# Kernel tuning notes

Measured on AMD Instinct MI355X. Metric: run time of the kernel, lower is better.

Reference implementation:

```python
import jax, jax.numpy as jnp
import numpy as np

B, T, S, H, E = 128, 32, 256, 1024, 1024


def setup_inputs() -> dict:
    key = jax.random.key(0)
    ks = jax.random.split(key, 8)
    sc = lambda n: 1.0 / np.sqrt(n)
    return dict(
        dec_seq=jax.random.normal(ks[0], (B, T, E), jnp.float32),      # embedded decoder inputs
        enc_hiddens=jax.random.normal(ks[1], (B, S, H), jnp.float32),  # encoder outputs
        last_hidden=jax.random.normal(ks[2], (B, H), jnp.float32),     # initial decoder state
        W_att=jax.random.normal(ks[3], (2 * H, H), jnp.float32) * sc(2 * H),  # concat-score W
        V_att=jax.random.normal(ks[4], (H, 1), jnp.float32) * sc(H),          # concat-score V
        Wi=jax.random.normal(ks[5], (E + H, 3 * H), jnp.float32) * sc(E + H),  # GRU input kernel (z,r,h)
        Uh=jax.random.normal(ks[6], (H, 3 * H), jnp.float32) * sc(H),          # GRU recurrent kernel
        b=jnp.zeros((3 * H,), jnp.float32),                                    # GRU bias
    )


def reference(dec_seq, enc_hiddens, last_hidden, W_att, V_att, Wi, Uh, b):
    Bn, Sn, Hn = enc_hiddens.shape

    def step(h, x_t):
        # Bahdanau 'concat' score: tanh([h; enc] @ W) @ V -> softmax over source
        hid = jnp.broadcast_to(h[:, None, :], (Bn, Sn, Hn))
        combined = jnp.concatenate([hid, enc_hiddens], axis=2)          # [B,S,2H]
        score = jnp.tanh(jnp.einsum('bsk,kh->bsh', combined, W_att))    # [B,S,H]
        score = jnp.einsum('bsh,h->bs', score, V_att[:, 0])             # [B,S]
        attn = jax.nn.softmax(score, axis=-1)
        context = jnp.einsum('bs,bsh->bh', attn, enc_hiddens)           # [B,H]
        # GRU cell on concat([x_t, context])
        inp = jnp.concatenate([x_t, context], axis=1)                   # [B,E+H]
        gz, gr, gh = jnp.split(inp @ Wi + b, 3, axis=1)
        rz, rr, rh = jnp.split(h @ Uh, 3, axis=1)
        z = jax.nn.sigmoid(gz + rz)
        r = jax.nn.sigmoid(gr + rr)
        hh = jnp.tanh(gh + r * rh)
        h_new = z * h + (1.0 - z) * hh
        return h_new, h_new

    _, outs = jax.lax.scan(step, last_hidden, jnp.swapaxes(dec_seq, 0, 1))
    return jnp.swapaxes(outs, 0, 1)  # [B,T,H]
```

## Files before the change

### kernel.cpp

```cpp
#include <hip/hip_runtime.h>
#include <hip/hip_bf16.h>
#include <stdint.h>

#define B_ 128
#define T_ 32
#define S_ 256
#define H_ 1024
#define E_ 1024
#define LOG2E 1.4426950408889634f

typedef __attribute__((ext_vector_type(8))) short short8;
typedef __attribute__((ext_vector_type(4))) float f32x4;
typedef __attribute__((ext_vector_type(2))) float f32x2;

typedef const __attribute__((address_space(1))) unsigned int* gas_ptr;
typedef __attribute__((address_space(3))) unsigned int* las_ptr;

__device__ __forceinline__ void gl_lds16(const void* g, void* l) {
    __builtin_amdgcn_global_load_lds((gas_ptr)g, (las_ptr)l, 16, 0, 0);
}

__device__ __forceinline__ float bf2f(unsigned short u) {
    union { unsigned int i; float f; } v; v.i = ((unsigned int)u) << 16; return v.f;
}
__device__ __forceinline__ unsigned short f2bf(float f) {
    union { float f; unsigned int i; } v; v.f = f;
    unsigned int i = v.i;
    return (unsigned short)((i + 0x7FFFu + ((i >> 16) & 1u)) >> 16);
}
__device__ __forceinline__ unsigned char f2fp8(float f) {
    return (unsigned char)((unsigned int)__builtin_amdgcn_cvt_pk_fp8_f32(f, f, 0, false) & 0xFF);
}
__device__ __forceinline__ float fexp2(float x) { return __builtin_amdgcn_exp2f(x); }
__device__ __forceinline__ float frcp(float x)  { return __builtin_amdgcn_rcpf(x); }
__device__ __forceinline__ float fast_tanh(float x) {
    float e = fexp2(x * (2.0f * LOG2E));
    return 1.0f - 2.0f * frcp(e + 1.0f);
}
__device__ __forceinline__ float fast_sigmoid(float x) {
    return frcp(1.0f + fexp2(-LOG2E * x));
}

__global__ __launch_bounds__(256) void conv_bf16(const float* __restrict__ src,
                                                 unsigned short* __restrict__ dst, long n) {
    long i = ((long)blockIdx.x * 256 + threadIdx.x) * 8;
    if (i >= n) return;
    float4 x = *(const float4*)(src + i);
    float4 y = *(const float4*)(src + i + 4);
    unsigned int w0 = (unsigned int)f2bf(x.x) | ((unsigned int)f2bf(x.y) << 16);
    unsigned int w1 = (unsigned int)f2bf(x.z) | ((unsigned int)f2bf(x.w) << 16);
    unsigned int w2 = (unsigned int)f2bf(y.x) | ((unsigned int)f2bf(y.y) << 16);
    unsigned int w3 = (unsigned int)f2bf(y.z) | ((unsigned int)f2bf(y.w) << 16);
    uint4 o; o.x = w0; o.y = w1; o.z = w2; o.w = w3;
    *(uint4*)(dst + i) = o;
}

__global__ __launch_bounds__(256) void conv_fp8(const float* __restrict__ src,
                                                unsigned char* __restrict__ dst, long n) {
    long i = ((long)blockIdx.x * 256 + threadIdx.x) * 8;
    if (i >= n) return;
    float4 x = *(const float4*)(src + i);
    float4 y = *(const float4*)(src + i + 4);
    unsigned int w0 = (unsigned int)__builtin_amdgcn_cvt_pk_fp8_f32(x.x, x.y, 0, false);
    w0 = (unsigned int)__builtin_amdgcn_cvt_pk_fp8_f32(x.z, x.w, (int)w0, true);
    unsigned int w1 = (unsigned int)__builtin_amdgcn_cvt_pk_fp8_f32(y.x, y.y, 0, false);
    w1 = (unsigned int)__builtin_amdgcn_cvt_pk_fp8_f32(y.z, y.w, (int)w1, true);
    uint2 o; o.x = w0; o.y = w1;
    *(uint2*)(dst + i) = o;
}

__global__ __launch_bounds__(256) void init_h(const float* __restrict__ h0,
                                              float* __restrict__ hbuf,
                                              unsigned short* __restrict__ hbf, int n) {
    int i = blockIdx.x * 256 + threadIdx.x;
    if (i < n) { float v = h0[i]; hbuf[i] = v; hbf[i] = f2bf(v); }
}

__global__ __launch_bounds__(256) void transpose_conv(const float* __restrict__ src, int ldsrc,
                                                      unsigned short* __restrict__ dst, int lddst,
                                                      float scale) {
    __shared__ float tile[64][65];
    int tid = threadIdx.x;
    int c0 = blockIdx.x * 64, r0 = blockIdx.y * 64;
    int tr = tid >> 6, tc = tid & 63;
#pragma unroll
    for (int i = 0; i < 16; i++) {
        int r = i * 4 + tr;
        tile[r][tc] = src[(long)(r0 + r) * ldsrc + c0 + tc];
    }
    __syncthreads();
#pragma unroll
    for (int i = 0; i < 16; i++) {
        int rr = i * 4 + tr;
        dst[(long)(c0 + rr) * lddst + r0 + tc] = f2bf(scale * tile[tc][rr]);
    }
}

__global__ __launch_bounds__(256) void transpose_conv_fp8(const float* __restrict__ src, int ldsrc,
                                                          unsigned char* __restrict__ dst, int lddst,
                                                          float scale) {
    __shared__ float tile[64][65];
    int tid = threadIdx.x;
    int c0 = blockIdx.x * 64, r0 = blockIdx.y * 64;
    int tr = tid >> 6, tc = tid & 63;
#pragma unroll
    for (int i = 0; i < 16; i++) {
        int r = i * 4 + tr;
        tile[r][tc] = src[(long)(r0 + r) * ldsrc + c0 + tc];
    }
    __syncthreads();
#pragma unroll
    for (int i = 0; i < 16; i++) {
        int rr = i * 4 + tr;
        dst[(long)(c0 + rr) * lddst + r0 + tc] = f2fp8(scale * tile[tc][rr]);
    }
}

template <int EPIL, int SWZ>
__global__ __launch_bounds__(256) void gemm128(const unsigned short* __restrict__ A, int lda,
                                               const unsigned short* __restrict__ Bt, int ldb,
                                               void* __restrict__ Cout, int ldc,
                                               int kLen, long partStride) {
    __shared__ unsigned short As[128 * 32];
    __shared__ unsigned short Bs[128 * 32];
    const int tid = threadIdx.x;
    int lin = blockIdx.y * gridDim.x + blockIdx.x;
    if (SWZ) {
        int cpx = (gridDim.x * gridDim.y) >> 3;
        lin = (lin & 7) * cpx + (lin >> 3);
    }
    const int n0 = (lin % gridDim.x) * 128;
    const int m0 = (lin / gridDim.x) * 128;
    const int kStart = blockIdx.z * kLen;
    const int w = tid >> 6, l = tid & 63;
    const int wr = w >> 1, wc = w & 1;

    f32x4 acc[4][4];
#pragma unroll
    for (int i = 0; i < 4; i++)
#pragma unroll
        for (int j = 0; j < 4; j++) acc[i][j] = f32x4{0.f, 0.f, 0.f, 0.f};

    for (int kt = 0; kt < kLen; kt += 32) {
        int k0 = kStart + kt;
#pragma unroll
        for (int i = 0; i < 2; i++) {
            int f = i * 4096 + tid * 16;
            int row = f >> 6;
            int cb = f & 63;
            gl_lds16(A + (long)(m0 + row) * lda + k0 + (cb >> 1), (char*)As + f);
            gl_lds16(Bt + (long)(n0 + row) * ldb + k0 + (cb >> 1), (char*)Bs + f);
        }
        asm volatile("s_waitcnt vmcnt(0)" ::: "memory");
        __syncthreads();
        short8 a[4], b[4];
#pragma unroll
        for (int fi = 0; fi < 4; fi++) {
            a[fi] = *(const short8*)((const char*)As + ((wr * 64 + fi * 16 + (l & 15)) * 32 + ((l >> 4) * 8)) * 2);
            b[fi] = *(const short8*)((const char*)Bs + ((wc * 64 + fi * 16 + (l & 15)) * 32 + ((l >> 4) * 8)) * 2);
        }
#pragma unroll
        for (int fi = 0; fi < 4; fi++)
#pragma unroll
            for (int fj = 0; fj < 4; fj++)
                acc[fi][fj] = __builtin_amdgcn_mfma_f32_16x16x32_bf16(a[fi], b[fj], acc[fi][fj], 0, 0, 0);
        __syncthreads();
    }

    long cz = (long)blockIdx.z * partStride;
#pragma unroll
    for (int fi = 0; fi < 4; fi++)
#pragma unroll
        for (int fj = 0; fj < 4; fj++) {
            int m = m0 + wr * 64 + fi * 16 + ((l >> 4) << 2);
            int n = n0 + wc * 64 + fj * 16 + (l & 15);
#pragma unroll
            for (int r = 0; r < 4; r++)
                ((unsigned short*)Cout + cz)[(long)(m + r) * ldc + n] = f2bf(acc[fi][fj][r]);
        }
}

template <int SWZ>
__global__ __launch_bounds__(256) void gemm128_f8(const unsigned char* __restrict__ A, int lda,
                                                  const unsigned char* __restrict__ Bt, int ldb,
                                                  unsigned char* __restrict__ Cout, int ldc,
                                                  int kLen) {
    __shared__ unsigned char As[128 * 64];
    __shared__ unsigned char Bs[128 * 64];
    const int tid = threadIdx.x;
    int lin = blockIdx.y * gridDim.x + blockIdx.x;
    if (SWZ) {
        int cpx = (gridDim.x * gridDim.y) >> 3;
        lin = (lin & 7) * cpx + (lin >> 3);
    }
    const int n0 = (lin % gridDim.x) * 128;
    const int m0 = (lin / gridDim.x) * 128;
    const int w = tid >> 6, l = tid & 63;
    const int wr = w >> 1, wc = w & 1;
    const int sx = (l & 6) << 3;

    f32x4 acc[4][4];
#pragma unroll
    for (int i = 0; i < 4; i++)
#pragma unroll
        for (int j = 0; j < 4; j++) acc[i][j] = f32x4{0.f, 0.f, 0.f, 0.f};

    for (int k0 = 0; k0 < kLen; k0 += 64) {
#pragma unroll
        for (int i = 0; i < 2; i++) {
            int f = i * 4096 + tid * 16;
            int row = f >> 6;
            int cb = (f & 63) ^ ((row & 6) << 3);
            gl_lds16(A + (long)(m0 + row) * lda + k0 + cb, (char*)As + f);
            gl_lds16(Bt + (long)(n0 + row) * ldb + k0 + cb, (char*)Bs + f);
        }
        asm volatile("s_waitcnt vmcnt(0)" ::: "memory");
        __syncthreads();
        long a[4][2], b[4][2];
#pragma unroll
        for (int fi = 0; fi < 4; fi++)
#pragma unroll
            for (int ks = 0; ks < 2; ks++) {
                int colb = (ks * 32 + ((l >> 4) * 8)) ^ sx;
                a[fi][ks] = *(const long*)(As + (wr * 64 + fi * 16 + (l & 15)) * 64 + colb);
                b[fi][ks] = *(const long*)(Bs + (wc * 64 + fi * 16 + (l & 15)) * 64 + colb);
            }
#pragma unroll
        for (int fi = 0; fi < 4; fi++)
#pragma unroll
            for (int fj = 0; fj < 4; fj++) {
                acc[fi][fj] = __builtin_amdgcn_mfma_f32_16x16x32_fp8_fp8(a[fi][0], b[fj][0], acc[fi][fj], 0, 0, 0);
                acc[fi][fj] = __builtin_amdgcn_mfma_f32_16x16x32_fp8_fp8(a[fi][1], b[fj][1], acc[fi][fj], 0, 0, 0);
            }
        __syncthreads();
    }

#pragma unroll
    for (int fi = 0; fi < 4; fi++)
#pragma unroll
        for (int fj = 0; fj < 4; fj++) {
            int m = m0 + wr * 64 + fi * 16 + ((l >> 4) << 2);
            int n = n0 + wc * 64 + fj * 16 + (l & 15);
#pragma unroll
            for (int r = 0; r < 4; r++)
                Cout[(long)(m + r) * ldc + n] = f2fp8(acc[fi][fj][r]);
        }
}

__global__ __launch_bounds__(256) void recgates(const unsigned short* __restrict__ hbf,
                                                const unsigned short* __restrict__ ctxbf,
                                                const unsigned short* __restrict__ Uht,
                                                const unsigned short* __restrict__ Wit2,
                                                unsigned short* __restrict__ gpart) {
    __shared__ unsigned short As[128 * 32];
    __shared__ unsigned short Bs[128 * 32];
    const int tid = threadIdx.x;
    const int n0 = blockIdx.x * 128;
    const int y = blockIdx.y, z = blockIdx.z;
    const unsigned short* A  = y ? ctxbf : hbf;
    const unsigned short* Bt = y ? Wit2 : Uht;
    const int kStart = z * 256;
    const int w = tid >> 6, l = tid & 63;
    const int wr = w >> 1, wc = w & 1;

    f32x4 acc[4][4];
#pragma unroll
    for (int i = 0; i < 4; i++)
#pragma unroll
        for (int j = 0; j < 4; j++) acc[i][j] = f32x4{0.f, 0.f, 0.f, 0.f};

    for (int kt = 0; kt < 256; kt += 32) {
        int k0 = kStart + kt;
#pragma unroll
        for (int i = 0; i < 2; i++) {
            int f = i * 4096 + tid * 16;
            int row = f >> 6;
            int cb = f & 63;
            gl_lds16(A + (long)row * 1024 + k0 + (cb >> 1), (char*)As + f);
            gl_lds16(Bt + (long)(n0 + row) * 1024 + k0 + (cb >> 1), (char*)Bs + f);
        }
        asm volatile("s_waitcnt vmcnt(0)" ::: "memory");
        __syncthreads();
        short8 a[4], b[4];
#pragma unroll
        for (int fi = 0; fi < 4; fi++) {
            a[fi] = *(const short8*)((const char*)As + ((wr * 64 + fi * 16 + (l & 15)) * 32 + ((l >> 4) * 8)) * 2);
            b[fi] = *(const short8*)((const char*)Bs + ((wc * 64 + fi * 16 + (l & 15)) * 32 + ((l >> 4) * 8)) * 2);
        }
#pragma unroll
        for (int fi = 0; fi < 4; fi++)
#pragma unroll
            for (int fj = 0; fj < 4; fj++)
                acc[fi][fj] = __builtin_amdgcn_mfma_f32_16x16x32_bf16(a[fi], b[fj], acc[fi][fj], 0, 0, 0);
        __syncthreads();
    }

    unsigned short* C = gpart + (long)(y * 4 + z) * (128 * 3072);
#pragma unroll
    for (int fi = 0; fi < 4; fi++)
#pragma unroll
        for (int fj = 0; fj < 4; fj++) {
            int m = wr * 64 + fi * 16 + ((l >> 4) << 2);
            int n = n0 + wc * 64 + fj * 16 + (l & 15);
#pragma unroll
            for (int r = 0; r < 4; r++)
                C[(long)(m + r) * 3072 + n] = f2bf(acc[fi][fj][r]);
        }
}

__global__ __launch_bounds__(256) void attn_kernel(const unsigned char* __restrict__ P8,
                                                   const unsigned char* __restrict__ enc8,
                                                   const unsigned short* __restrict__ partq,
                                                   const float* __restrict__ V,
                                                   float* __restrict__ pctx,
                                                   float* __restrict__ pml) {
    const int oct = blockIdx.x, b = blockIdx.y;
    const int tid = threadIdx.x, w = tid >> 6, l = tid & 63;
    __shared__ float qs[1024];
    __shared__ float sc[32];
    __shared__ float wgt[32];

    {
        int j = tid * 4;
        float s0 = 0.f, s1 = 0.f, s2 = 0.f, s3 = 0.f;
#pragma unroll
        for (int p = 0; p < 8; p++) {
            ushort4 v = *(const ushort4*)(partq + (long)p * (128 * 1024) + (long)b * 1024 + j);
            s0 += bf2f(v.x); s1 += bf2f(v.y); s2 += bf2f(v.z); s3 += bf2f(v.w);
        }
        qs[j] = s0; qs[j + 1] = s1; qs[j + 2] = s2; qs[j + 3] = s3;
    }
    __syncthreads();

    float q[16], nv2[16];
    float sv = 0.f;
#pragma unroll
    for (int ii = 0; ii < 4; ii++) {
        float4 qq = *(const float4*)(qs + l * 16 + ii * 4);
        float4 vv = *(const float4*)(V + l * 16 + ii * 4);
        q[ii * 4 + 0] = qq.x; q[ii * 4 + 1] = qq.y; q[ii * 4 + 2] = qq.z; q[ii * 4 + 3] = qq.w;
        nv2[ii * 4 + 0] = -2.f * vv.x; nv2[ii * 4 + 1] = -2.f * vv.y;
        nv2[ii * 4 + 2] = -2.f * vv.z; nv2[ii * 4 + 3] = -2.f * vv.w;
        sv += vv.x + vv.y + vv.z + vv.w;
    }

    const int s0 = oct * 32;
#pragma unroll 2
    for (int ss = 0; ss < 8; ss++) {
        int s = w * 8 + ss;
        const unsigned char* prow = P8 + ((long)(b * S_ + s0 + s)) * H_ + l * 16;
        uint4 pw = *(const uint4*)prow;
        float pv[16];
        {
            f32x2 d;
            d = __builtin_amdgcn_cvt_pk_f32_fp8(pw.x, false); pv[0] = d.x; pv[1] = d.y;
            d = __builtin_amdgcn_cvt_pk_f32_fp8(pw.x, true);  pv[2] = d.x; pv[3] = d.y;
            d = __builtin_amdgcn_cvt_pk_f32_fp8(pw.y, false); pv[4] = d.x; pv[5] = d.y;
            d = __builtin_amdgcn_cvt_pk_f32_fp8(pw.y, true);  pv[6] = d.x; pv[7] = d.y;
            d = __builtin_amdgcn_cvt_pk_f32_fp8(pw.z, false); pv[8] = d.x; pv[9] = d.y;
            d = __builtin_amdgcn_cvt_pk_f32_fp8(pw.z, true);  pv[10] = d.x; pv[11] = d.y;
            d = __builtin_amdgcn_cvt_pk_f32_fp8(pw.w, false); pv[12] = d.x; pv[13] = d.y;
            d = __builtin_amdgcn_cvt_pk_f32_fp8(pw.w, true);  pv[14] = d.x; pv[15] = d.y;
        }
        float acc = sv;
#pragma unroll
        for (int i = 0; i < 16; i++) {
            float x = q[i] + pv[i];
            float d = frcp(fexp2(x) + 1.0f);
            acc = fmaf(d, nv2[i], acc);
        }
#pragma unroll
        for (int off = 32; off; off >>= 1) acc += __shfl_xor(acc, off);
        if (l == 0) sc[s] = acc;
    }
    __syncthreads();

    float v = (l < 32) ? sc[l] : -3.4e38f;
    float mx = v;
#pragma unroll
    for (int off = 32; off; off >>= 1) mx = fmaxf(mx, __shfl_xor(mx, off));
    float ex = (l < 32) ? fexp2((v - mx) * LOG2E) : 0.f;
    float ls = ex;
#pragma unroll
    for (int off = 32; off; off >>= 1) ls += __shfl_xor(ls, off);
    if (tid < 32) wgt[tid] = ex;
    if (tid == 0) {
        pml[(oct * 128 + b) * 2 + 0] = mx;
        pml[(oct * 128 + b) * 2 + 1] = ls;
    }
    __syncthreads();

    float a0 = 0.f, a1 = 0.f, a2 = 0.f, a3 = 0.f;
    const unsigned char* ebase = enc8 + ((long)(b * S_ + s0)) * H_ + tid * 4;
#pragma unroll 4
    for (int s = 0; s < 32; s++) {
        float ws = wgt[s];
        unsigned int u = *(const unsigned int*)(ebase + (long)s * H_);
        f32x2 lo = __builtin_amdgcn_cvt_pk_f32_fp8(u, false);
        f32x2 hi = __builtin_amdgcn_cvt_pk_f32_fp8(u, true);
        a0 = fmaf(ws, lo.x, a0);
        a1 = fmaf(ws, lo.y, a1);
        a2 = fmaf(ws, hi.x, a2);
        a3 = fmaf(ws, hi.y, a3);
    }
    float* po = pctx + ((long)(oct * 128 + b)) * H_ + tid * 4;
    po[0] = a0; po[1] = a1; po[2] = a2; po[3] = a3;
}

__global__ __launch_bounds__(256) void combine_ctx(const float* __restrict__ pctx,
                                                   const float* __restrict__ pml,
                                                   unsigned short* __restrict__ ctxbf) {
    int b = blockIdx.x, tid = threadIdx.x;
    float mm[8], ll[8];
    float m = -3.4e38f;
#pragma unroll
    for (int p = 0; p < 8; p++) {
        mm[p] = pml[(p * 128 + b) * 2 + 0];
        ll[p] = pml[(p * 128 + b) * 2 + 1];
        m = fmaxf(m, mm[p]);
    }
    float denom = 0.f, f[8];
#pragma unroll
    for (int p = 0; p < 8; p++) { f[p] = fexp2((mm[p] - m) * LOG2E); denom += f[p] * ll[p]; }
    float inv = frcp(denom);
    float a0 = 0.f, a1 = 0.f, a2 = 0.f, a3 = 0.f;
#pragma unroll
    for (int p = 0; p < 8; p++) {
        float4 c = *(const float4*)(pctx + ((long)(p * 128 + b)) * H_ + tid * 4);
        a0 = fmaf(f[p], c.x, a0); a1 = fmaf(f[p], c.y, a1);
        a2 = fmaf(f[p], c.z, a2); a3 = fmaf(f[p], c.w, a3);
    }
    unsigned short* o = ctxbf + (long)b * H_ + tid * 4;
    o[0] = f2bf(a0 * inv); o[1] = f2bf(a1 * inv); o[2] = f2bf(a2 * inv); o[3] = f2bf(a3 * inv);
}

__global__ __launch_bounds__(256) void gru_update(const unsigned short* __restrict__ gpart,
                                                  const unsigned short* __restrict__ xg,
                                                  const float* __restrict__ bias,
                                                  float* __restrict__ hbuf,
                                                  unsigned short* __restrict__ hbf,
                                                  float* __restrict__ out, int t) {
    const int m = blockIdx.x;
    const int j = threadIdx.x * 4;
    const unsigned short* xr = xg + ((long)(m * T_ + t)) * 3072;
    ushort4 xz = *(const ushort4*)(xr + j);
    ushort4 xrr = *(const ushort4*)(xr + 1024 + j);
    ushort4 xh = *(const ushort4*)(xr + 2048 + j);
    float gz[4] = {bf2f(xz.x), bf2f(xz.y), bf2f(xz.z), bf2f(xz.w)};
    float gr[4] = {bf2f(xrr.x), bf2f(xrr.y), bf2f(xrr.z), bf2f(xrr.w)};
    float gh[4] = {bf2f(xh.x), bf2f(xh.y), bf2f(xh.z), bf2f(xh.w)};
    float rz[4] = {0, 0, 0, 0}, rr[4] = {0, 0, 0, 0}, rh[4] = {0, 0, 0, 0};
#pragma unroll
    for (int p = 0; p < 8; p++) {
        const unsigned short* gp = gpart + (long)p * (128 * 3072) + (long)m * 3072;
        ushort4 a = *(const ushort4*)(gp + j);
        ushort4 bb = *(const ushort4*)(gp + 1024 + j);
        ushort4 c = *(const ushort4*)(gp + 2048 + j);
        if (p < 4) {
            rz[0] += bf2f(a.x); rz[1] += bf2f(a.y); rz[2] += bf2f(a.z); rz[3] += bf2f(a.w);
            rr[0] += bf2f(bb.x); rr[1] += bf2f(bb.y); rr[2] += bf2f(bb.z); rr[3] += bf2f(bb.w);
            rh[0] += bf2f(c.x); rh[1] += bf2f(c.y); rh[2] += bf2f(c.z); rh[3] += bf2f(c.w);
        } else {
            gz[0] += bf2f(a.x); gz[1] += bf2f(a.y); gz[2] += bf2f(a.z); gz[3] += bf2f(a.w);
            gr[0] += bf2f(bb.x); gr[1] += bf2f(bb.y); gr[2] += bf2f(bb.z); gr[3] += bf2f(bb.w);
            gh[0] += bf2f(c.x); gh[1] += bf2f(c.y); gh[2] += bf2f(c.z); gh[3] += bf2f(c.w);
        }
    }
    float4 bz = *(const float4*)(bias + j);
    float4 br = *(const float4*)(bias + 1024 + j);
    float4 bh = *(const float4*)(bias + 2048 + j);
    float4 hv = *(const float4*)(hbuf + (long)m * H_ + j);
    float bzf[4] = {bz.x, bz.y, bz.z, bz.w};
    float brf[4] = {br.x, br.y, br.z, br.w};
    float bhf[4] = {bh.x, bh.y, bh.z, bh.w};
    float hf[4] = {hv.x, hv.y, hv.z, hv.w};
    float hn[4];
    ushort4 hb;
#pragma unroll
    for (int c = 0; c < 4; c++) {
        float z = fast_sigmoid(gz[c] + bzf[c] + rz[c]);
        float r = fast_sigmoid(gr[c] + brf[c] + rr[c]);
        float hh = fast_tanh(gh[c] + bhf[c] + r * rh[c]);
        hn[c] = z * hf[c] + (1.0f - z) * hh;
    }
    hb.x = f2bf(hn[0]); hb.y = f2bf(hn[1]); hb.z = f2bf(hn[2]); hb.w = f2bf(hn[3]);
    float4 ho; ho.x = hn[0]; ho.y = hn[1]; ho.z = hn[2]; ho.w = hn[3];
    *(float4*)(out + ((long)m * T_ + t) * H_ + j) = ho;
    *(float4*)(hbuf + (long)m * H_ + j) = ho;
    *(ushort4*)(hbf + (long)m * H_ + j) = hb;
}

__global__ void sentinel_k(float* out) {
    if (threadIdx.x == 0 && blockIdx.x == 0) out[0] = 1.2345e8f;
}

extern "C" void kernel_launch(void* const* d_in, const int* in_sizes, int n_in,
                              void* d_out, int out_size, void* d_ws, size_t ws_size,
                              hipStream_t stream) {
    const float* dec  = (const float*)d_in[0];
    const float* enc  = (const float*)d_in[1];
    const float* h0   = (const float*)d_in[2];
    const float* Watt = (const float*)d_in[3];
    const float* Vatt = (const float*)d_in[4];
    const float* Wi   = (const float*)d_in[5];
    const float* Uh   = (const float*)d_in[6];
    const float* bias = (const float*)d_in[7];
    float* out = (float*)d_out;

    char* ws = (char*)d_ws;
    size_t off = 0;
    auto alloc = [&](size_t bytes) -> void* {
        void* p = ws + off;
        off += (bytes + 255) & ~(size_t)255;
        return p;
    };
    unsigned char*  P8    = (unsigned char*)alloc((size_t)32768 * 1024);
    unsigned char*  enc8  = (unsigned char*)alloc((size_t)33554432);
    unsigned short* decbf = (unsigned short*)alloc((size_t)4194304 * 2);
    unsigned short* Xg    = (unsigned short*)alloc((size_t)4096 * 3072 * 2);
    unsigned short* Wit1  = (unsigned short*)alloc((size_t)3072 * 1024 * 2);
    unsigned short* Wit2  = (unsigned short*)alloc((size_t)3072 * 1024 * 2);
    unsigned short* Uht   = (unsigned short*)alloc((size_t)3072 * 1024 * 2);
    unsigned short* W1t   = (unsigned short*)alloc((size_t)1024 * 1024 * 2);
    unsigned char*  W2t8  = (unsigned char*)alloc((size_t)1024 * 1024);
    unsigned short* partq = (unsigned short*)alloc((size_t)8 * 128 * 1024 * 2);
    unsigned short* gpart = (unsigned short*)alloc((size_t)8 * 128 * 3072 * 2);
    float* pctx  = (float*)alloc((size_t)8 * 128 * 1024 * 4);
    float* pml   = (float*)alloc((size_t)8 * 128 * 2 * 4);
    unsigned short* ctxbf = (unsigned short*)alloc((size_t)128 * 1024 * 2);
    float* hbuf  = (float*)alloc((size_t)128 * 1024 * 4);
    unsigned short* hbf = (unsigned short*)alloc((size_t)128 * 1024 * 2);

    if (off > ws_size) {
        sentinel_k<<<1, 64, 0, stream>>>(out);
        return;
    }

    const float qscale = 2.0f * LOG2E;

    conv_fp8<<<33554432 / 8 / 256, 256, 0, stream>>>(enc, enc8, 33554432);
    conv_bf16<<<4194304 / 8 / 256, 256, 0, stream>>>(dec, decbf, 4194304);
    init_h<<<512, 256, 0, stream>>>(h0, hbuf, hbf, 131072);
    transpose_conv<<<dim3(48, 16), 256, 0, stream>>>(Wi, 3072, Wit1, 1024, 1.0f);
    transpose_conv<<<dim3(48, 16), 256, 0, stream>>>(Wi + (size_t)1024 * 3072, 3072, Wit2, 1024, 1.0f);
    transpose_conv<<<dim3(48, 16), 256, 0, stream>>>(Uh, 3072, Uht, 1024, 1.0f);
    transpose_conv<<<dim3(16, 16), 256, 0, stream>>>(Watt, 1024, W1t, 1024, qscale);
    transpose_conv_fp8<<<dim3(16, 16), 256, 0, stream>>>(Watt + (size_t)1024 * 1024, 1024, W2t8, 1024, qscale);
    gemm128_f8<1><<<dim3(8, 256, 1), 256, 0, stream>>>(enc8, 1024, W2t8, 1024, P8, 1024, 1024);
    gemm128<0, 1><<<dim3(24, 32, 1), 256, 0, stream>>>(decbf, 1024, Wit1, 1024, Xg, 3072, 1024, 0);

    for (int t = 0; t < T_; t++) {
        gemm128<0, 0><<<dim3(8, 1, 8), 256, 0, stream>>>(hbf, 1024, W1t, 1024, partq, 1024, 128,
                                                         (long)128 * 1024);
        attn_kernel<<<dim3(8, 128), 256, 0, stream>>>(P8, enc8, partq, Vatt, pctx, pml);
        combine_ctx<<<128, 256, 0, stream>>>(pctx, pml, ctxbf);
        recgates<<<dim3(24, 2, 4), 256, 0, stream>>>(hbf, ctxbf, Uht, Wit2, gpart);
        gru_update<<<128, 256, 0, stream>>>(gpart, Xg, bias, hbuf, hbf, out, t);
    }
}
```

Baseline: 1.402 ms.

## Fuse h-dependent attention query and GRU recurrent GEMMs into one launch

Concatenates the transposed attention W1 and the GRU recurrent kernel Uh into one [4096x1024] weight so a single GEMM on the hidden state produces both the attention query and the recurrent gate pre-activations. The recurrent half of the old recgates kernel moves off the serial path after attention; the remaining ctxgates kernel now only handles the context-dependent input gates. Split-K for the query drops from 8 to 4 partials, and the fused GEMM launches 128 blocks instead of 64. The larger fused GEMM now sits before attention, so that stage does more work per step.

```diff
diff --git a/kernel.cpp b/kernel.cpp
--- a/kernel.cpp
+++ b/kernel.cpp
@@ -116,10 +116,10 @@
     }
 }
 
-template <int EPIL, int SWZ>
+template <int SWZ>
 __global__ __launch_bounds__(256) void gemm128(const unsigned short* __restrict__ A, int lda,
                                                const unsigned short* __restrict__ Bt, int ldb,
-                                               void* __restrict__ Cout, int ldc,
+                                               unsigned short* __restrict__ Cout, int ldc,
                                                int kLen, long partStride) {
     __shared__ unsigned short As[128 * 32];
     __shared__ unsigned short Bs[128 * 32];
@@ -176,7 +176,7 @@
             int n = n0 + wc * 64 + fj * 16 + (l & 15);
 #pragma unroll
             for (int r = 0; r < 4; r++)
-                ((unsigned short*)Cout + cz)[(long)(m + r) * ldc + n] = f2bf(acc[fi][fj][r]);
+                (Cout + cz)[(long)(m + r) * ldc + n] = f2bf(acc[fi][fj][r]);
         }
 }
 
@@ -247,18 +247,14 @@
         }
 }
 
-__global__ __launch_bounds__(256) void recgates(const unsigned short* __restrict__ hbf,
-                                                const unsigned short* __restrict__ ctxbf,
-                                                const unsigned short* __restrict__ Uht,
+__global__ __launch_bounds__(256) void ctxgates(const unsigned short* __restrict__ ctxbf,
                                                 const unsigned short* __restrict__ Wit2,
-                                                unsigned short* __restrict__ gpart) {
+                                                unsigned short* __restrict__ cpart) {
     __shared__ unsigned short As[128 * 32];
     __shared__ unsigned short Bs[128 * 32];
     const int tid = threadIdx.x;
     const int n0 = blockIdx.x * 128;
-    const int y = blockIdx.y, z = blockIdx.z;
-    const unsigned short* A  = y ? ctxbf : hbf;
-    const unsigned short* Bt = y ? Wit2 : Uht;
+    const int z = blockIdx.z;
     const int kStart = z * 256;
     const int w = tid >> 6, l = tid & 63;
     const int wr = w >> 1, wc = w & 1;
@@ -276,8 +272,8 @@
             int f = i * 4096 + tid * 16;
             int row = f >> 6;
             int cb = f & 63;
-            gl_lds16(A + (long)row * 1024 + k0 + (cb >> 1), (char*)As + f);
-            gl_lds16(Bt + (long)(n0 + row) * 1024 + k0 + (cb >> 1), (char*)Bs + f);
+            gl_lds16(ctxbf + (long)row * 1024 + k0 + (cb >> 1), (char*)As + f);
+            gl_lds16(Wit2 + (long)(n0 + row) * 1024 + k0 + (cb >> 1), (char*)Bs + f);
         }
         asm volatile("s_waitcnt vmcnt(0)" ::: "memory");
         __syncthreads();
@@ -295,7 +291,7 @@
         __syncthreads();
     }
 
-    unsigned short* C = gpart + (long)(y * 4 + z) * (128 * 3072);
+    unsigned short* C = cpart + (long)z * (128 * 3072);
 #pragma unroll
     for (int fi = 0; fi < 4; fi++)
 #pragma unroll
@@ -310,7 +306,7 @@
 
 __global__ __launch_bounds__(256) void attn_kernel(const unsigned char* __restrict__ P8,
                                                    const unsigned char* __restrict__ enc8,
-                                                   const unsigned short* __restrict__ partq,
+                                                   const unsigned short* __restrict__ hpart,
                                                    const float* __restrict__ V,
                                                    float* __restrict__ pctx,
                                                    float* __restrict__ pml) {
@@ -324,8 +320,8 @@
         int j = tid * 4;
         float s0 = 0.f, s1 = 0.f, s2 = 0.f, s3 = 0.f;
 #pragma unroll
-        for (int p = 0; p < 8; p++) {
-            ushort4 v = *(const ushort4*)(partq + (long)p * (128 * 1024) + (long)b * 1024 + j);
+        for (int p = 0; p < 4; p++) {
+            ushort4 v = *(const ushort4*)(hpart + (long)p * (128 * 4096) + (long)b * 4096 + j);
             s0 += bf2f(v.x); s1 += bf2f(v.y); s2 += bf2f(v.z); s3 += bf2f(v.w);
         }
         qs[j] = s0; qs[j + 1] = s1; qs[j + 2] = s2; qs[j + 3] = s3;
@@ -434,7 +430,8 @@
     o[0] = f2bf(a0 * inv); o[1] = f2bf(a1 * inv); o[2] = f2bf(a2 * inv); o[3] = f2bf(a3 * inv);
 }
 
-__global__ __launch_bounds__(256) void gru_update(const unsigned short* __restrict__ gpart,
+__global__ __launch_bounds__(256) void gru_update(const unsigned short* __restrict__ cpart,
+                                                  const unsigned short* __restrict__ hpart,
                                                   const unsigned short* __restrict__ xg,
                                                   const float* __restrict__ bias,
                                                   float* __restrict__ hbuf,
@@ -451,20 +448,24 @@
     float gh[4] = {bf2f(xh.x), bf2f(xh.y), bf2f(xh.z), bf2f(xh.w)};
     float rz[4] = {0, 0, 0, 0}, rr[4] = {0, 0, 0, 0}, rh[4] = {0, 0, 0, 0};
 #pragma unroll
-    for (int p = 0; p < 8; p++) {
-        const unsigned short* gp = gpart + (long)p * (128 * 3072) + (long)m * 3072;
+    for (int p = 0; p < 4; p++) {
+        const unsigned short* hp = hpart + (long)p * (128 * 4096) + (long)m * 4096;
+        ushort4 a = *(const ushort4*)(hp + 1024 + j);
+        ushort4 bb = *(const ushort4*)(hp + 2048 + j);
+        ushort4 c = *(const ushort4*)(hp + 3072 + j);
+        rz[0] += bf2f(a.x); rz[1] += bf2f(a.y); rz[2] += bf2f(a.z); rz[3] += bf2f(a.w);
+        rr[0] += bf2f(bb.x); rr[1] += bf2f(bb.y); rr[2] += bf2f(bb.z); rr[3] += bf2f(bb.w);
+        rh[0] += bf2f(c.x); rh[1] += bf2f(c.y); rh[2] += bf2f(c.z); rh[3] += bf2f(c.w);
+    }
+#pragma unroll
+    for (int p = 0; p < 4; p++) {
+        const unsigned short* gp = cpart + (long)p * (128 * 3072) + (long)m * 3072;
         ushort4 a = *(const ushort4*)(gp + j);
         ushort4 bb = *(const ushort4*)(gp + 1024 + j);
         ushort4 c = *(const ushort4*)(gp + 2048 + j);
-        if (p < 4) {
-            rz[0] += bf2f(a.x); rz[1] += bf2f(a.y); rz[2] += bf2f(a.z); rz[3] += bf2f(a.w);
-            rr[0] += bf2f(bb.x); rr[1] += bf2f(bb.y); rr[2] += bf2f(bb.z); rr[3] += bf2f(bb.w);
-            rh[0] += bf2f(c.x); rh[1] += bf2f(c.y); rh[2] += bf2f(c.z); rh[3] += bf2f(c.w);
-        } else {
-            gz[0] += bf2f(a.x); gz[1] += bf2f(a.y); gz[2] += bf2f(a.z); gz[3] += bf2f(a.w);
-            gr[0] += bf2f(bb.x); gr[1] += bf2f(bb.y); gr[2] += bf2f(bb.z); gr[3] += bf2f(bb.w);
-            gh[0] += bf2f(c.x); gh[1] += bf2f(c.y); gh[2] += bf2f(c.z); gh[3] += bf2f(c.w);
-        }
+        gz[0] += bf2f(a.x); gz[1] += bf2f(a.y); gz[2] += bf2f(a.z); gz[3] += bf2f(a.w);
+        gr[0] += bf2f(bb.x); gr[1] += bf2f(bb.y); gr[2] += bf2f(bb.z); gr[3] += bf2f(bb.w);
+        gh[0] += bf2f(c.x); gh[1] += bf2f(c.y); gh[2] += bf2f(c.z); gh[3] += bf2f(c.w);
     }
     float4 bz = *(const float4*)(bias + j);
     float4 br = *(const float4*)(bias + 1024 + j);
@@ -520,11 +521,10 @@
     unsigned short* Xg    = (unsigned short*)alloc((size_t)4096 * 3072 * 2);
     unsigned short* Wit1  = (unsigned short*)alloc((size_t)3072 * 1024 * 2);
     unsigned short* Wit2  = (unsigned short*)alloc((size_t)3072 * 1024 * 2);
-    unsigned short* Uht   = (unsigned short*)alloc((size_t)3072 * 1024 * 2);
-    unsigned short* W1t   = (unsigned short*)alloc((size_t)1024 * 1024 * 2);
+    unsigned short* U4t   = (unsigned short*)alloc((size_t)4096 * 1024 * 2);
     unsigned char*  W2t8  = (unsigned char*)alloc((size_t)1024 * 1024);
-    unsigned short* partq = (unsigned short*)alloc((size_t)8 * 128 * 1024 * 2);
-    unsigned short* gpart = (unsigned short*)alloc((size_t)8 * 128 * 3072 * 2);
+    unsigned short* hpart = (unsigned short*)alloc((size_t)4 * 128 * 4096 * 2);
+    unsigned short* cpart = (unsigned short*)alloc((size_t)4 * 128 * 3072 * 2);
     float* pctx  = (float*)alloc((size_t)8 * 128 * 1024 * 4);
     float* pml   = (float*)alloc((size_t)8 * 128 * 2 * 4);
     unsigned short* ctxbf = (unsigned short*)alloc((size_t)128 * 1024 * 2);
@@ -543,18 +543,18 @@
     init_h<<<512, 256, 0, stream>>>(h0, hbuf, hbf, 131072);
     transpose_conv<<<dim3(48, 16), 256, 0, stream>>>(Wi, 3072, Wit1, 1024, 1.0f);
     transpose_conv<<<dim3(48, 16), 256, 0, stream>>>(Wi + (size_t)1024 * 3072, 3072, Wit2, 1024, 1.0f);
-    transpose_conv<<<dim3(48, 16), 256, 0, stream>>>(Uh, 3072, Uht, 1024, 1.0f);
-    transpose_conv<<<dim3(16, 16), 256, 0, stream>>>(Watt, 1024, W1t, 1024, qscale);
+    transpose_conv<<<dim3(16, 16), 256, 0, stream>>>(Watt, 1024, U4t, 1024, qscale);
+    transpose_conv<<<dim3(48, 16), 256, 0, stream>>>(Uh, 3072, U4t + (size_t)1024 * 1024, 1024, 1.0f);
     transpose_conv_fp8<<<dim3(16, 16), 256, 0, stream>>>(Watt + (size_t)1024 * 1024, 1024, W2t8, 1024, qscale);
     gemm128_f8<1><<<dim3(8, 256, 1), 256, 0, stream>>>(enc8, 1024, W2t8, 1024, P8, 1024, 1024);
-    gemm128<0, 1><<<dim3(24, 32, 1), 256, 0, stream>>>(decbf, 1024, Wit1, 1024, Xg, 3072, 1024, 0);
+    gemm128<1><<<dim3(24, 32, 1), 256, 0, stream>>>(decbf, 1024, Wit1, 1024, Xg, 3072, 1024, 0);
 
     for (int t = 0; t < T_; t++) {
-        gemm128<0, 0><<<dim3(8, 1, 8), 256, 0, stream>>>(hbf, 1024, W1t, 1024, partq, 1024, 128,
-                                                         (long)128 * 1024);
-        attn_kernel<<<dim3(8, 128), 256, 0, stream>>>(P8, enc8, partq, Vatt, pctx, pml);
+        gemm128<0><<<dim3(32, 1, 4), 256, 0, stream>>>(hbf, 1024, U4t, 1024, hpart, 4096, 256,
+                                                       (long)128 * 4096);
+        attn_kernel<<<dim3(8, 128), 256, 0, stream>>>(P8, enc8, hpart, Vatt, pctx, pml);
         combine_ctx<<<128, 256, 0, stream>>>(pctx, pml, ctxbf);
-        recgates<<<dim3(24, 2, 4), 256, 0, stream>>>(hbf, ctxbf, Uht, Wit2, gpart);
-        gru_update<<<128, 256, 0, stream>>>(gpart, Xg, bias, hbuf, hbf, out, t);
-    }
-}
+        ctxgates<<<dim3(24, 1, 4), 256, 0, stream>>>(ctxbf, Wit2, cpart);
+        gru_update<<<128, 256, 0, stream>>>(cpart, hpart, Xg, bias, hbuf, hbf, out, t);
+    }
+}
```

Result: slower. 1.449 ms (+3.3%).
